# Optimization experiments

Hardware: AMD Instinct MI355X
Metric: run time of the kernel (lower is better)

The kernel has to match this reference:

```python
import jax, jax.numpy as jnp
import numpy as np

NUM_HEADS = 8
HEAD_SIZE = 64  # hidden_dim // num_heads = 512 // 8
SCALE = 1.0 / np.sqrt(HEAD_SIZE).astype(np.float32)
CAUSAL = True


def setup_inputs() -> dict:
    key = jax.random.key(0)
    k1, k2, k3 = jax.random.split(key, 3)
    b, s, d = 4, 2048, 512
    x = jax.random.normal(k1, (b, s, d), dtype=jnp.float32)
    w_qkv = jax.random.normal(k2, (d, 3 * d), dtype=jnp.float32) * 0.02
    b_qkv = jnp.zeros((3 * d,), dtype=jnp.float32)
    w_out = jax.random.normal(k3, (d, d), dtype=jnp.float32) * 0.02
    b_out = jnp.zeros((d,), dtype=jnp.float32)
    return {"x": x, "w_qkv": w_qkv, "b_qkv": b_qkv, "w_out": w_out, "b_out": b_out}


def reference(x, w_qkv, b_qkv, w_out, b_out):
    b, s, d = x.shape
    h, hd = NUM_HEADS, HEAD_SIZE
    qkv = x @ w_qkv + b_qkv                      # (b, s, 3d)
    q, k, v = jnp.split(qkv, 3, axis=-1)
    # (b, s, d) -> (b, h, s, hd)
    q = q.reshape(b, s, h, hd).transpose(0, 2, 1, 3)
    k = k.reshape(b, s, h, hd).transpose(0, 2, 1, 3)
    v = v.reshape(b, s, h, hd).transpose(0, 2, 1, 3)
    scores = jnp.einsum('bhqd,bhkd->bhqk', q, k) * SCALE  # (b, h, s, s)
    if CAUSAL:
        causal_mask = jnp.triu(jnp.ones((s, s), dtype=bool), k=1)
        scores = jnp.where(causal_mask, -jnp.inf, scores)
    attn = jax.nn.softmax(scores, axis=-1)
    out = jnp.einsum('bhqk,bhkd->bhqd', attn, v)          # (b, h, s, hd)
    out = out.transpose(0, 2, 1, 3).reshape(b, s, d)
    return out @ w_out + b_out
```

## Files before the change

kernel.cpp:

```cpp
#include <hip/hip_runtime.h>
#include <hip/hip_bf16.h>

#define BATCH 4
#define SEQ   2048
#define DM    512
#define NH    8
#define HD    64
#define PART  (BATCH*NH*SEQ*HD)
#define QSCALE 0.18033688f

typedef unsigned short u16;
typedef unsigned int   u32;
typedef __bf16 bf16x8 __attribute__((ext_vector_type(8)));
typedef float  f32x4  __attribute__((ext_vector_type(4)));

__device__ __forceinline__ u16 f2bf(float f) {
    union { float f; u32 u; } v; v.f = f;
    u32 r = v.u + 0x7fffu + ((v.u >> 16) & 1u);
    return (u16)(r >> 16);
}

__device__ __forceinline__ void glds16(const u16* g, u16* lds) {
    __builtin_amdgcn_global_load_lds(
        (const __attribute__((address_space(1))) void*)g,
        (__attribute__((address_space(3))) void*)lds, 16, 0, 0);
}

__global__ __launch_bounds__(256) void prep_k(
    const float* __restrict__ x, u16* __restrict__ xb,
    const float* __restrict__ w_qkv, u16* __restrict__ t_qkv,
    const float* __restrict__ w_out, u16* __restrict__ t_out)
{
    __shared__ u16 Ts[64][72];
    const int z = blockIdx.z, bx = blockIdx.x, t = threadIdx.x;

    if (z == 0) {
        const int n8 = PART / 8;
        for (int i = bx * 256 + t; i < n8; i += 512 * 256) {
            float4 a = *(const float4*)(x + (size_t)i * 8);
            float4 b = *(const float4*)(x + (size_t)i * 8 + 4);
            union { uint4 v; u16 s[8]; } o;
            o.s[0] = f2bf(a.x); o.s[1] = f2bf(a.y);
            o.s[2] = f2bf(a.z); o.s[3] = f2bf(a.w);
            o.s[4] = f2bf(b.x); o.s[5] = f2bf(b.y);
            o.s[6] = f2bf(b.z); o.s[7] = f2bf(b.w);
            *(uint4*)(xb + (size_t)i * 8) = o.v;
        }
        return;
    }
    const int N = (z == 1) ? 3 * DM : DM;
    const int ntiles = N / 64;
    if (bx >= ntiles * 8) return;
    const float* W = (z == 1) ? w_qkv : w_out;
    u16* Wt = (z == 1) ? t_qkv : t_out;
    const int n0 = (bx % ntiles) * 64, k0 = (bx / ntiles) * 64;

    #pragma unroll
    for (int l = 0; l < 4; ++l) {
        int idx = l * 1024 + t * 4;
        int r = idx >> 6, c = idx & 63;
        float4 v = *(const float4*)(W + (size_t)(k0 + r) * N + n0 + c);
        Ts[c + 0][r] = f2bf(v.x);
        Ts[c + 1][r] = f2bf(v.y);
        Ts[c + 2][r] = f2bf(v.z);
        Ts[c + 3][r] = f2bf(v.w);
    }
    __syncthreads();
    #pragma unroll
    for (int l = 0; l < 2; ++l) {
        int idx = l * 256 + t;
        int row = idx >> 3, ch = idx & 7;
        *(uint4*)(Wt + (size_t)(n0 + row) * DM + k0 + ch * 8) =
            *(const uint4*)(&Ts[row][ch * 8]);
    }
}

template<int MODE>
__global__ __launch_bounds__(256) void gemm_k(
    const u16* __restrict__ A, const u16* __restrict__ Bt,
    const float* __restrict__ bias, void* __restrict__ outv,
    int M, int N, int K)
{
    constexpr int BM = (MODE == 1) ? 64 : 128;
    constexpr int NI = (MODE == 1) ? 2 : 4;

    __shared__ __align__(16) u16 As[2][BM * 32];
    __shared__ __align__(16) u16 Bs[2][128 * 32];

    const int tid  = threadIdx.x;
    const int bm0  = blockIdx.x * BM;
    const int bn0  = blockIdx.y * 128;
    const int wave = tid >> 6, lane = tid & 63;
    const int l16  = lane & 15, quad = lane >> 4;
    const int wr   = (MODE == 1) ? 0 : (wave & 1) * 64;
    const int wc   = (MODE == 1) ? wave * 32 : (wave >> 1) * 64;

    const int srow = (lane >> 2);
    const int scol = (lane & 3) * 8;
    const int arow = (MODE == 1) ? (wave * 16) : (wave * 32);
    const u16* Ag = A + (size_t)(bm0 + arow + srow) * K + scol;
    const u16* Bg = Bt + (size_t)(bn0 + wave * 32 + srow) * K + scol;
    const int wofsA = arow * 32;
    const int wofsB = (wave * 32) * 32;

    f32x4 acc[4][NI];
    #pragma unroll
    for (int i = 0; i < 4; ++i)
        #pragma unroll
        for (int j = 0; j < NI; ++j)
            acc[i][j] = (f32x4){0.f, 0.f, 0.f, 0.f};

    glds16(Ag, &As[0][wofsA]);
    if (MODE == 0) glds16(Ag + (size_t)16 * K, &As[0][wofsA + 16 * 32]);
    glds16(Bg,                  &Bs[0][wofsB]);
    glds16(Bg + (size_t)16 * K, &Bs[0][wofsB + 16 * 32]);
    __syncthreads();

    const int NIT = K >> 5;
    for (int it = 0; it < NIT; ++it) {
        const int cur = it & 1;
        if (it + 1 < NIT) {
            const int nx = cur ^ 1;
            const int k0 = (it + 1) << 5;
            glds16(Ag + k0, &As[nx][wofsA]);
            if (MODE == 0) glds16(Ag + k0 + (size_t)16 * K, &As[nx][wofsA + 16 * 32]);
            glds16(Bg + k0,                  &Bs[nx][wofsB]);
            glds16(Bg + k0 + (size_t)16 * K, &Bs[nx][wofsB + 16 * 32]);
        }

        bf16x8 af[4], bfr[NI];
        #pragma unroll
        for (int mi = 0; mi < 4; ++mi)
            af[mi] = *(const bf16x8*)(&As[cur][(wr + mi * 16 + l16) * 32 + quad * 8]);
        #pragma unroll
        for (int ni = 0; ni < NI; ++ni)
            bfr[ni] = *(const bf16x8*)(&Bs[cur][(wc + ni * 16 + l16) * 32 + quad * 8]);
        #pragma unroll
        for (int mi = 0; mi < 4; ++mi)
            #pragma unroll
            for (int ni = 0; ni < NI; ++ni)
                acc[mi][ni] = __builtin_amdgcn_mfma_f32_16x16x32_bf16(
                    af[mi], bfr[ni], acc[mi][ni], 0, 0, 0);
        __syncthreads();
    }

    #pragma unroll
    for (int mi = 0; mi < 4; ++mi) {
        #pragma unroll
        for (int ni = 0; ni < NI; ++ni) {
            int col = bn0 + wc + ni * 16 + l16;
            float bv = bias[col];
            int row0 = bm0 + wr + mi * 16 + quad * 4;
            float v[4];
            #pragma unroll
            for (int reg = 0; reg < 4; ++reg) v[reg] = acc[mi][ni][reg] + bv;

            if (MODE == 1) {
                #pragma unroll
                for (int reg = 0; reg < 4; ++reg)
                    ((float*)outv)[(size_t)(row0 + reg) * N + col] = v[reg];
            } else {
                u16* ws = (u16*)outv;
                int part = col >> 9, wi = col & 511;
                int h = wi >> 6, e = wi & 63;
                int b = row0 >> 11, s0 = row0 & 2047;
                if (part == 2) {
                    union { u16 q[4]; uint2 u; } pk;
                    #pragma unroll
                    for (int reg = 0; reg < 4; ++reg) pk.q[reg] = f2bf(v[reg]);
                    *(uint2*)(ws + (size_t)2 * PART +
                              ((size_t)(b * NH + h) * HD + e) * SEQ + s0) = pk.u;
                } else {
                    float scl = (part == 0) ? QSCALE : 1.0f;
                    #pragma unroll
                    for (int reg = 0; reg < 4; ++reg)
                        ws[(size_t)part * PART +
                           ((size_t)(b * NH + h) * SEQ + s0 + reg) * HD + e] =
                            f2bf(v[reg] * scl);
                }
            }
        }
    }
}

__global__ __launch_bounds__(256) void attn_k(
    const u16* __restrict__ Q, const u16* __restrict__ K,
    const u16* __restrict__ Vt, u16* __restrict__ O)
{
    __shared__ __align__(16) u16 KsB[2][64 * 64];
    __shared__ __align__(16) u16 VtB[2][64 * 64];
    __shared__ __align__(16) u16 Ps[64][72];

    const int bh = blockIdx.x;
    const int pair = blockIdx.y;
    const int tid = threadIdx.x, wave = tid >> 6, lane = tid & 63;
    const int l16 = lane & 15, quad = lane >> 4;
    const size_t baseK = (size_t)bh * SEQ * HD;
    const size_t baseV = (size_t)bh * HD * SEQ;
    const int b = bh >> 3, h = bh & 7;
    const int row64 = wave * 16 + quad * 4;

    const int sub = lane >> 3;
    const int lcx = (lane & 7) ^ sub;
    const u16* kg = K  + baseK + (size_t)((wave * 16 + sub) * 64)   + lcx * 8;
    const u16* vg = Vt + baseV + (size_t)((wave * 16 + sub) * 2048) + lcx * 8;
    u16* ksd = &KsB[0][wave * 1024];
    u16* vtd = &VtB[0][wave * 1024];

    #pragma unroll
    for (int phase = 0; phase < 2; ++phase) {
        const int qt = phase ? pair : (31 - pair);
        const size_t baseQ = baseK + (size_t)qt * 64 * HD;

        #pragma unroll
        for (int r = 0; r < 2; ++r) {
            int chunk = r * 256 + tid;
            int row = chunk >> 3, c8 = (chunk & 7) << 3;
            *(uint4*)(&Ps[row][c8]) = *(const uint4*)(Q + baseQ + row * 64 + c8);
        }
        __syncthreads();
        bf16x8 qf[2];
        #pragma unroll
        for (int d0 = 0; d0 < 2; ++d0)
            qf[d0] = *(const bf16x8*)(&Ps[wave * 16 + l16][d0 * 32 + quad * 8]);
        __syncthreads();

        glds16(kg,            ksd);
        glds16(kg + 8 * 64,   ksd + 512);
        glds16(vg,            vtd);
        glds16(vg + 8 * 2048, vtd + 512);
        __syncthreads();

        float l_part[4] = {0.f, 0.f, 0.f, 0.f};
        f32x4 o_acc[4];
        #pragma unroll
        for (int i = 0; i < 4; ++i) o_acc[i] = (f32x4){0.f, 0.f, 0.f, 0.f};

        for (int kt = 0; kt <= qt; ++kt) {
            const int cur = kt & 1;
            if (kt < qt) {
                const int nx = (cur ^ 1) * 4096;
                glds16(kg + (size_t)(kt + 1) * 4096,          ksd + nx);
                glds16(kg + (size_t)(kt + 1) * 4096 + 8 * 64, ksd + nx + 512);
                glds16(vg + (size_t)(kt + 1) * 64,            vtd + nx);
                glds16(vg + (size_t)(kt + 1) * 64 + 8 * 2048, vtd + nx + 512);
            }

            bf16x8 kf[2][4], vf[2][4];
            #pragma unroll
            for (int d0 = 0; d0 < 2; ++d0)
                #pragma unroll
                for (int nt = 0; nt < 4; ++nt) {
                    int pc = (d0 * 4 + quad) ^ (l16 & 7);
                    kf[d0][nt] = *(const bf16x8*)
                        (&KsB[cur][(nt * 16 + l16) * 64 + pc * 8]);
                    vf[d0][nt] = *(const bf16x8*)
                        (&VtB[cur][(nt * 16 + l16) * 64 + pc * 8]);
                }

            f32x4 s[4];
            #pragma unroll
            for (int nt = 0; nt < 4; ++nt) s[nt] = (f32x4){0.f, 0.f, 0.f, 0.f};
            #pragma unroll
            for (int d0 = 0; d0 < 2; ++d0)
                #pragma unroll
                for (int nt = 0; nt < 4; ++nt)
                    s[nt] = __builtin_amdgcn_mfma_f32_16x16x32_bf16(
                        qf[d0], kf[d0][nt], s[nt], 0, 0, 0);

            const bool diag = (kt == qt);
            #pragma unroll
            for (int nt = 0; nt < 4; ++nt) {
                int cl = nt * 16 + l16;
                float p[4];
                #pragma unroll
                for (int reg = 0; reg < 4; ++reg) {
                    p[reg] = __builtin_amdgcn_exp2f(s[nt][reg]);
                    if (diag && cl > row64 + reg) p[reg] = 0.f;
                    l_part[reg] += p[reg];
                }
                union { __hip_bfloat162 hh; u16 s2[2]; } pk01, pk23;
                pk01.hh = __float22bfloat162_rn(float2{p[0], p[1]});
                pk23.hh = __float22bfloat162_rn(float2{p[2], p[3]});
                Ps[row64 + 0][cl] = pk01.s2[0];
                Ps[row64 + 1][cl] = pk01.s2[1];
                Ps[row64 + 2][cl] = pk23.s2[0];
                Ps[row64 + 3][cl] = pk23.s2[1];
            }

            #pragma unroll
            for (int k0 = 0; k0 < 2; ++k0) {
                bf16x8 ap = *(const bf16x8*)
                    (&Ps[wave * 16 + l16][k0 * 32 + quad * 8]);
                #pragma unroll
                for (int dt = 0; dt < 4; ++dt)
                    o_acc[dt] = __builtin_amdgcn_mfma_f32_16x16x32_bf16(
                        ap, vf[k0][dt], o_acc[dt], 0, 0, 0);
            }
            __syncthreads();
        }

        float l_i[4];
        #pragma unroll
        for (int reg = 0; reg < 4; ++reg) {
            float l = l_part[reg];
            #pragma unroll
            for (int off = 1; off < 16; off <<= 1)
                l += __shfl_xor(l, off);
            l_i[reg] = l;
        }
        #pragma unroll
        for (int dt = 0; dt < 4; ++dt) {
            #pragma unroll
            for (int reg = 0; reg < 4; ++reg) {
                int srow = qt * 64 + row64 + reg;
                float v = o_acc[dt][reg] / l_i[reg];
                size_t idx = (((size_t)(b * SEQ + srow)) * NH + h) * HD
                             + dt * 16 + l16;
                O[idx] = f2bf(v);
            }
        }
    }
}

extern "C" void kernel_launch(void* const* d_in, const int* in_sizes, int n_in,
                              void* d_out, int out_size, void* d_ws, size_t ws_size,
                              hipStream_t stream) {
    const float* x     = (const float*)d_in[0];
    const float* w_qkv = (const float*)d_in[1];
    const float* b_qkv = (const float*)d_in[2];
    const float* w_out = (const float*)d_in[3];
    const float* b_out = (const float*)d_in[4];

    u16* qkv    = (u16*)d_ws;
    u16* attn   = qkv + (size_t)3 * PART;
    u16* xb     = attn + (size_t)PART;
    u16* wt_qkv = xb + (size_t)PART;
    u16* wt_out = wt_qkv + (size_t)(3 * DM) * DM;

    const int M = BATCH * SEQ;

    prep_k<<<dim3(512, 1, 3), 256, 0, stream>>>(x, xb, w_qkv, wt_qkv,
                                                w_out, wt_out);

    dim3 g1(M / 128, (3 * DM) / 128);
    gemm_k<0><<<g1, 256, 0, stream>>>(xb, wt_qkv, b_qkv, qkv, M, 3 * DM, DM);

    dim3 g2(BATCH * NH, 16);
    attn_k<<<g2, 256, 0, stream>>>(qkv, qkv + PART, qkv + 2 * (size_t)PART, attn);

    dim3 g3(M / 64, DM / 128);
    gemm_k<1><<<g3, 256, 0, stream>>>(attn, wt_out, b_out, (float*)d_out, M, DM, DM);
}
```

Measured before the change: 150.9 us.

## Use 32x32 MFMA with register-resident P via permlane32 swap and KV-split waves

Restructures the attention kernel so each wave computes a 32x32 query-by-key tile with 32x32x16 bf16 MFMA. The P matrix stays in registers, rearranged with permlane32_swap instead of a round-trip through LDS, and the waves split the key dimension in half with a final cross-wave reduction through shared memory. Diagonal tiles where the key half lies entirely above the query half are skipped, and launch bounds request two blocks per CU. This removes the Ps LDS traffic and improves MFMA efficiency, at the cost of an extra LDS partial-output reduction and more live registers.

```diff
diff --git a/kernel.cpp b/kernel.cpp
--- a/kernel.cpp
+++ b/kernel.cpp
@@ -13,6 +13,8 @@
 typedef unsigned int   u32;
 typedef __bf16 bf16x8 __attribute__((ext_vector_type(8)));
 typedef float  f32x4  __attribute__((ext_vector_type(4)));
+typedef float  f32x16 __attribute__((ext_vector_type(16)));
+typedef unsigned int u32x2 __attribute__((ext_vector_type(2)));
 
 __device__ __forceinline__ u16 f2bf(float f) {
     union { float f; u32 u; } v; v.f = f;
@@ -24,6 +26,11 @@
     __builtin_amdgcn_global_load_lds(
         (const __attribute__((address_space(1))) void*)g,
         (__attribute__((address_space(3))) void*)lds, 16, 0, 0);
+}
+
+__device__ __forceinline__ void pl32swap(u32 &a, u32 &b) {
+    u32x2 r = __builtin_amdgcn_permlane32_swap(a, b, false, false);
+    a = r[0]; b = r[1];
 }
 
 __global__ __launch_bounds__(256) void prep_k(
@@ -183,22 +190,22 @@
     }
 }
 
-__global__ __launch_bounds__(256) void attn_k(
+__global__ __launch_bounds__(256, 2) void attn_k(
     const u16* __restrict__ Q, const u16* __restrict__ K,
     const u16* __restrict__ Vt, u16* __restrict__ O)
 {
     __shared__ __align__(16) u16 KsB[2][64 * 64];
     __shared__ __align__(16) u16 VtB[2][64 * 64];
-    __shared__ __align__(16) u16 Ps[64][72];
-
-    const int bh = blockIdx.x;
+    __shared__ float Lred[4][32];
+
+    const int bh   = blockIdx.x;
     const int pair = blockIdx.y;
     const int tid = threadIdx.x, wave = tid >> 6, lane = tid & 63;
-    const int l16 = lane & 15, quad = lane >> 4;
+    const int l31 = lane & 31, hi = lane >> 5, x7 = lane & 7;
+    const int qh = wave >> 1, kh = wave & 1;
     const size_t baseK = (size_t)bh * SEQ * HD;
     const size_t baseV = (size_t)bh * HD * SEQ;
     const int b = bh >> 3, h = bh & 7;
-    const int row64 = wave * 16 + quad * 4;
 
     const int sub = lane >> 3;
     const int lcx = (lane & 7) ^ sub;
@@ -207,22 +214,26 @@
     u16* ksd = &KsB[0][wave * 1024];
     u16* vtd = &VtB[0][wave * 1024];
 
+    int koff[4], voff[2][2];
+    #pragma unroll
+    for (int k = 0; k < 4; ++k)
+        koff[k] = (kh * 32 + l31) * 64 + ((((k << 1) + hi)) ^ x7) * 8;
+    #pragma unroll
+    for (int dt = 0; dt < 2; ++dt)
+        #pragma unroll
+        for (int k0 = 0; k0 < 2; ++k0)
+            voff[dt][k0] = (dt * 32 + l31) * 64 + ((kh * 4 + k0 * 2 + hi) ^ x7) * 8;
+
     #pragma unroll
     for (int phase = 0; phase < 2; ++phase) {
         const int qt = phase ? pair : (31 - pair);
-        const size_t baseQ = baseK + (size_t)qt * 64 * HD;
-
-        #pragma unroll
-        for (int r = 0; r < 2; ++r) {
-            int chunk = r * 256 + tid;
-            int row = chunk >> 3, c8 = (chunk & 7) << 3;
-            *(uint4*)(&Ps[row][c8]) = *(const uint4*)(Q + baseQ + row * 64 + c8);
-        }
-        __syncthreads();
-        bf16x8 qf[2];
-        #pragma unroll
-        for (int d0 = 0; d0 < 2; ++d0)
-            qf[d0] = *(const bf16x8*)(&Ps[wave * 16 + l16][d0 * 32 + quad * 8]);
+
+        const u16* qg = Q + baseK + (size_t)(qt * 64 + qh * 32 + l31) * 64 + hi * 8;
+        bf16x8 qf[4];
+        #pragma unroll
+        for (int k = 0; k < 4; ++k)
+            qf[k] = *(const bf16x8*)(qg + k * 16);
+
         __syncthreads();
 
         glds16(kg,            ksd);
@@ -231,10 +242,10 @@
         glds16(vg + 8 * 2048, vtd + 512);
         __syncthreads();
 
-        float l_part[4] = {0.f, 0.f, 0.f, 0.f};
-        f32x4 o_acc[4];
-        #pragma unroll
-        for (int i = 0; i < 4; ++i) o_acc[i] = (f32x4){0.f, 0.f, 0.f, 0.f};
+        float la0 = 0.f, la1 = 0.f;
+        f32x16 o0, o1;
+        #pragma unroll
+        for (int i = 0; i < 16; ++i) { o0[i] = 0.f; o1[i] = 0.f; }
 
         for (int kt = 0; kt <= qt; ++kt) {
             const int cur = kt & 1;
@@ -246,78 +257,84 @@
                 glds16(vg + (size_t)(kt + 1) * 64 + 8 * 2048, vtd + nx + 512);
             }
 
-            bf16x8 kf[2][4], vf[2][4];
+            const bool diag = (kt == qt);
+            if (!(diag && kh > qh)) {
+                bf16x8 kf[4], vf[2][2];
+                #pragma unroll
+                for (int k = 0; k < 4; ++k)
+                    kf[k] = *(const bf16x8*)(&KsB[cur][koff[k]]);
+                #pragma unroll
+                for (int dt = 0; dt < 2; ++dt)
+                    #pragma unroll
+                    for (int k0 = 0; k0 < 2; ++k0)
+                        vf[dt][k0] = *(const bf16x8*)(&VtB[cur][voff[dt][k0]]);
+
+                f32x16 st;
+                #pragma unroll
+                for (int i = 0; i < 16; ++i) st[i] = 0.f;
+                #pragma unroll
+                for (int k = 0; k < 4; ++k)
+                    st = __builtin_amdgcn_mfma_f32_32x32x16_bf16(
+                        kf[k], qf[k], st, 0, 0, 0);
+
+                float p[16];
+                #pragma unroll
+                for (int r = 0; r < 16; ++r)
+                    p[r] = __builtin_amdgcn_exp2f(st[r]);
+                if (diag && kh == qh) {
+                    #pragma unroll
+                    for (int r = 0; r < 16; ++r) {
+                        int kvl = (r & 3) + 8 * (r >> 2) + 4 * hi;
+                        if (kvl > l31) p[r] = 0.f;
+                    }
+                }
+                #pragma unroll
+                for (int r = 0; r < 8; ++r) { la0 += p[r]; la1 += p[r + 8]; }
+
+                u32 c[8];
+                #pragma unroll
+                for (int m = 0; m < 8; ++m) {
+                    __hip_bfloat162 t =
+                        __float22bfloat162_rn(float2{p[2 * m], p[2 * m + 1]});
+                    c[m] = *(u32*)&t;
+                }
+                pl32swap(c[0], c[2]); pl32swap(c[1], c[3]);
+                pl32swap(c[4], c[6]); pl32swap(c[5], c[7]);
+                union { u32 w[4]; bf16x8 v; } pa0, pa1;
+                pa0.w[0] = c[0]; pa0.w[1] = c[1]; pa0.w[2] = c[2]; pa0.w[3] = c[3];
+                pa1.w[0] = c[4]; pa1.w[1] = c[5]; pa1.w[2] = c[6]; pa1.w[3] = c[7];
+
+                o0 = __builtin_amdgcn_mfma_f32_32x32x16_bf16(pa0.v, vf[0][0], o0, 0, 0, 0);
+                o0 = __builtin_amdgcn_mfma_f32_32x32x16_bf16(pa1.v, vf[0][1], o0, 0, 0, 0);
+                o1 = __builtin_amdgcn_mfma_f32_32x32x16_bf16(pa0.v, vf[1][0], o1, 0, 0, 0);
+                o1 = __builtin_amdgcn_mfma_f32_32x32x16_bf16(pa1.v, vf[1][1], o1, 0, 0, 0);
+            }
+            __syncthreads();
+        }
+
+        float l2 = (la0 + la1);
+        l2 += __shfl_xor(l2, 32);
+        if (lane < 32) Lred[wave][lane] = l2;
+        float* Ob = (qh == 0) ? (float*)&KsB[0][0] : (float*)&VtB[0][0];
+        if (kh == 1) {
             #pragma unroll
-            for (int d0 = 0; d0 < 2; ++d0)
-                #pragma unroll
-                for (int nt = 0; nt < 4; ++nt) {
-                    int pc = (d0 * 4 + quad) ^ (l16 & 7);
-                    kf[d0][nt] = *(const bf16x8*)
-                        (&KsB[cur][(nt * 16 + l16) * 64 + pc * 8]);
-                    vf[d0][nt] = *(const bf16x8*)
-                        (&VtB[cur][(nt * 16 + l16) * 64 + pc * 8]);
-                }
-
-            f32x4 s[4];
+            for (int r = 0; r < 16; ++r) {
+                Ob[r * 64 + lane]        = o0[r];
+                Ob[(16 + r) * 64 + lane] = o1[r];
+            }
+        }
+        __syncthreads();
+        if (kh == 0) {
             #pragma unroll
-            for (int nt = 0; nt < 4; ++nt) s[nt] = (f32x4){0.f, 0.f, 0.f, 0.f};
-            #pragma unroll
-            for (int d0 = 0; d0 < 2; ++d0)
-                #pragma unroll
-                for (int nt = 0; nt < 4; ++nt)
-                    s[nt] = __builtin_amdgcn_mfma_f32_16x16x32_bf16(
-                        qf[d0], kf[d0][nt], s[nt], 0, 0, 0);
-
-            const bool diag = (kt == qt);
-            #pragma unroll
-            for (int nt = 0; nt < 4; ++nt) {
-                int cl = nt * 16 + l16;
-                float p[4];
-                #pragma unroll
-                for (int reg = 0; reg < 4; ++reg) {
-                    p[reg] = __builtin_amdgcn_exp2f(s[nt][reg]);
-                    if (diag && cl > row64 + reg) p[reg] = 0.f;
-                    l_part[reg] += p[reg];
-                }
-                union { __hip_bfloat162 hh; u16 s2[2]; } pk01, pk23;
-                pk01.hh = __float22bfloat162_rn(float2{p[0], p[1]});
-                pk23.hh = __float22bfloat162_rn(float2{p[2], p[3]});
-                Ps[row64 + 0][cl] = pk01.s2[0];
-                Ps[row64 + 1][cl] = pk01.s2[1];
-                Ps[row64 + 2][cl] = pk23.s2[0];
-                Ps[row64 + 3][cl] = pk23.s2[1];
-            }
-
-            #pragma unroll
-            for (int k0 = 0; k0 < 2; ++k0) {
-                bf16x8 ap = *(const bf16x8*)
-                    (&Ps[wave * 16 + l16][k0 * 32 + quad * 8]);
-                #pragma unroll
-                for (int dt = 0; dt < 4; ++dt)
-                    o_acc[dt] = __builtin_amdgcn_mfma_f32_16x16x32_bf16(
-                        ap, vf[k0][dt], o_acc[dt], 0, 0, 0);
-            }
-            __syncthreads();
-        }
-
-        float l_i[4];
-        #pragma unroll
-        for (int reg = 0; reg < 4; ++reg) {
-            float l = l_part[reg];
-            #pragma unroll
-            for (int off = 1; off < 16; off <<= 1)
-                l += __shfl_xor(l, off);
-            l_i[reg] = l;
-        }
-        #pragma unroll
-        for (int dt = 0; dt < 4; ++dt) {
-            #pragma unroll
-            for (int reg = 0; reg < 4; ++reg) {
-                int srow = qt * 64 + row64 + reg;
-                float v = o_acc[dt][reg] / l_i[reg];
-                size_t idx = (((size_t)(b * SEQ + srow)) * NH + h) * HD
-                             + dt * 16 + l16;
-                O[idx] = f2bf(v);
+            for (int r = 0; r < 16; ++r) {
+                int ql = (r & 3) + 8 * (r >> 2) + 4 * hi;
+                float lt = Lred[2 * qh][ql] + Lred[2 * qh + 1][ql];
+                int srow = qt * 64 + qh * 32 + ql;
+                size_t idx = (((size_t)(b * SEQ + srow)) * NH + h) * HD + l31;
+                float v0 = (o0[r] + Ob[r * 64 + lane]) / lt;
+                float v1 = (o1[r] + Ob[(16 + r) * 64 + lane]) / lt;
+                O[idx]      = f2bf(v0);
+                O[idx + 32] = f2bf(v1);
             }
         }
     }
```

Result: faster. 146.5 us (-2.9%).
